# Kernel optimization log

Measured on AMD Instinct MI355X. Metric: run time of the kernel, lower is better.

Reference implementation:

```python
import jax, jax.numpy as jnp
import numpy as np

N, E, D, H, L, G = 50000, 800000, 128, 8, 3, 64
C = D // H  # per-head dim


def setup_inputs() -> dict:
    key = jax.random.key(0)
    ks = jax.random.split(key, 10)
    s = 1.0 / np.sqrt(D)  # glorot-ish scale
    return {
        "x": jax.random.normal(ks[0], (N, D), jnp.float32),
        "edge_index": jax.random.randint(ks[1], (2, E), 0, N, jnp.int32),
        "batch": jnp.sort(jax.random.randint(ks[2], (N,), 0, G, jnp.int32)),
        "Wq": jax.random.normal(ks[3], (L, D, D), jnp.float32) * s,
        "bq": jnp.zeros((L, D), jnp.float32),
        "Wk": jax.random.normal(ks[4], (L, D, D), jnp.float32) * s,
        "bk": jnp.zeros((L, D), jnp.float32),
        "Wv": jax.random.normal(ks[5], (L, D, D), jnp.float32) * s,
        "bv": jnp.zeros((L, D), jnp.float32),
        "Ws": jax.random.normal(ks[6], (L, D, D), jnp.float32) * s,
        "bs": jnp.zeros((L, D), jnp.float32),
        "w_gate": jax.random.normal(ks[7], (D, 1), jnp.float32) * s,
        "b_gate": jnp.zeros((1,), jnp.float32),
    }


def transformer_conv(x, src, dst, Wq, bq, Wk, bk, Wv, bv, Ws, bs):
    # PyG TransformerConv (concat=True, root_weight=True, no edge_attr, eval mode)
    n = x.shape[0]
    q = (x @ Wq + bq).reshape(n, H, C)
    k = (x @ Wk + bk).reshape(n, H, C)
    v = (x @ Wv + bv).reshape(n, H, C)
    # attention logits per edge: [E, H]
    alpha = jnp.einsum('ehc,ehc->eh', q[dst], k[src]) / np.sqrt(C).astype(np.float32)
    # segment softmax over incoming edges of each destination node
    amax = jax.ops.segment_max(alpha, dst, num_segments=n)          # [N, H]
    ea = jnp.exp(alpha - amax[dst])
    denom = jax.ops.segment_sum(ea, dst, num_segments=n)            # [N, H]
    attn = ea / (denom[dst] + 1e-16)                                # [E, H]
    msg = v[src] * attn[:, :, None]                                 # [E, H, C]
    out = jax.ops.segment_sum(msg, dst, num_segments=n).reshape(n, H * C)
    return out + x @ Ws + bs                                        # skip connection


def reference(x, edge_index, batch, Wq, bq, Wk, bk, Wv, bv, Ws, bs, w_gate, b_gate):
    src, dst = edge_index[0], edge_index[1]
    for l in range(L):
        x = transformer_conv(x, src, dst, Wq[l], bq[l], Wk[l], bk[l],
                             Wv[l], bv[l], Ws[l], bs[l])
    # ReadoutPhase: gated sum pool || max pool
    score = jax.nn.sigmoid(x @ w_gate + b_gate)                     # [N, 1]
    pool_sum = jax.ops.segment_sum(score * x, batch, num_segments=G)
    pool_max = jax.ops.segment_max(x, batch, num_segments=G)
    return jnp.concatenate([pool_sum, pool_max], axis=1)            # [G, 2D]
```

## Files before the change

### kernel.cpp

```cpp
#include <hip/hip_runtime.h>
#include <hip/hip_bf16.h>

#define NN 50000
#define EE 800000
#define GG 64
#define PCH 16
#define SCB ((NN + 255) / 256)

typedef __attribute__((ext_vector_type(8)))  short          s16x8;
typedef __attribute__((ext_vector_type(8)))  unsigned short u16x8;
typedef __attribute__((ext_vector_type(16))) float          f32x16;

union BFU { __hip_bfloat16 h; unsigned short u; };
__device__ __forceinline__ unsigned short f2bf(float f) {
    BFU b; b.h = __float2bfloat16(f); return b.u;
}
#define B2F_LO(u) __uint_as_float((u) << 16)
#define B2F_HI(u) __uint_as_float((u) & 0xffff0000u)
#define BF2F(us)  __uint_as_float(((unsigned)(us)) << 16)

__global__ __launch_bounds__(256) void hist_kernel(const int* __restrict__ dst,
                                                   int* __restrict__ counts) {
    int e = blockIdx.x * 256 + threadIdx.x;
    if (e < EE) atomicAdd(&counts[dst[e]], 1);
}

__global__ __launch_bounds__(256)
void block_scan(const int* __restrict__ counts, int* __restrict__ offsets,
                int* __restrict__ bsums) {
    __shared__ int sm[256];
    const int t = threadIdx.x;
    const int i = blockIdx.x * 256 + t;
    const int v = (i < NN) ? counts[i] : 0;
    sm[t] = v;
    __syncthreads();
    for (int off = 1; off < 256; off <<= 1) {
        int val = (t >= off) ? sm[t - off] : 0;
        __syncthreads();
        sm[t] += val;
        __syncthreads();
    }
    if (i < NN) offsets[i] = sm[t] - v;
    if (t == 255) bsums[blockIdx.x] = sm[255];
}

__global__ __launch_bounds__(256)
void scan_sums(int* __restrict__ bsums) {
    __shared__ int sm[256];
    const int t = threadIdx.x;
    const int v = (t < SCB) ? bsums[t] : 0;
    sm[t] = v;
    __syncthreads();
    for (int off = 1; off < 256; off <<= 1) {
        int val = (t >= off) ? sm[t - off] : 0;
        __syncthreads();
        sm[t] += val;
        __syncthreads();
    }
    if (t < SCB) bsums[t] = sm[t] - v;
}

__global__ __launch_bounds__(256)
void add_base(int* __restrict__ offsets, const int* __restrict__ bsums) {
    const int i = blockIdx.x * 256 + threadIdx.x;
    if (i < NN) offsets[i] += bsums[blockIdx.x];
    if (i == 0) offsets[NN] = EE;
}

__global__ __launch_bounds__(256) void scatter_kernel(const int* __restrict__ src,
                                                      const int* __restrict__ dst,
                                                      const int* __restrict__ offs,
                                                      int* __restrict__ cursor,
                                                      int* __restrict__ csrc) {
    int e = blockIdx.x * 256 + threadIdx.x;
    if (e < EE) {
        int dn = dst[e];
        int p = atomicAdd(&cursor[dn], 1);
        csrc[offs[dn] + p] = src[e];
    }
}

__global__ __launch_bounds__(256) void starts_kernel(const int* __restrict__ batch,
                                                     int* __restrict__ starts) {
    int i = blockIdx.x * 256 + threadIdx.x;
    if (i > NN) return;
    int b  = (i < NN) ? batch[i] : GG;
    int bp = (i == 0) ? -1 : batch[i - 1];
    for (int g = bp + 1; g <= b && g <= GG; ++g) starts[g] = i;
}

__global__ __launch_bounds__(256)
void deg_hist(const int* __restrict__ counts, int* __restrict__ dhist) {
    __shared__ int lh[256];
    const int t = threadIdx.x;
    lh[t] = 0;
    __syncthreads();
    const int i = blockIdx.x * 256 + t;
    if (i < NN) atomicAdd(&lh[min(counts[i], 255)], 1);
    __syncthreads();
    if (lh[t]) atomicAdd(&dhist[t], lh[t]);
}

__global__ __launch_bounds__(256)
void deg_scan(int* __restrict__ dhist) {
    __shared__ int sm[256];
    const int t = threadIdx.x;
    const int v = dhist[t];
    sm[t] = v;
    __syncthreads();
    for (int off = 1; off < 256; off <<= 1) {
        int val = (t >= off) ? sm[t - off] : 0;
        __syncthreads();
        sm[t] += val;
        __syncthreads();
    }
    dhist[t] = sm[t] - v;
}

__global__ __launch_bounds__(256)
void deg_scatter(const int* __restrict__ counts, const int* __restrict__ dbase,
                 int* __restrict__ dcur, int* __restrict__ perm) {
    __shared__ int lh[256];
    __shared__ int lb[256];
    const int t = threadIdx.x;
    lh[t] = 0;
    __syncthreads();
    const int i = blockIdx.x * 256 + t;
    int d = 0, r = 0;
    if (i < NN) {
        d = min(counts[i], 255);
        r = atomicAdd(&lh[d], 1);
    }
    __syncthreads();
    if (lh[t]) lb[t] = atomicAdd(&dcur[t], lh[t]);
    __syncthreads();
    if (i < NN) perm[dbase[d] + lb[d] + r] = i;
}

__global__ __launch_bounds__(256)
void prep_weights(const float* __restrict__ Wq, const float* __restrict__ Wk,
                  const float* __restrict__ Wv, const float* __restrict__ Ws,
                  unsigned short* __restrict__ wtbh, unsigned short* __restrict__ wtbl) {
    const int mat = blockIdx.x;
    const int l = mat >> 2, m = mat & 3;
    const float* W;
    switch (m) {
        case 0:  W = Wq; break;
        case 1:  W = Wk; break;
        case 2:  W = Wv; break;
        default: W = Ws; break;
    }
    W += (size_t)l * 16384;
    const int t = threadIdx.x;
    const int col = blockIdx.y * 16 + (t >> 4);
    const int kb  = (t & 15) * 8;
    u16x8 hi, lo;
    #pragma unroll
    for (int j = 0; j < 8; ++j) {
        float w = W[(kb + j) * 128 + col];
        unsigned short uh = f2bf(w);
        hi[j] = uh;
        lo[j] = f2bf(w - BF2F(uh));
    }
    const size_t o = (size_t)mat * 16384 + col * 128 + kb;
    *(u16x8*)(wtbh + o) = hi;
    *(u16x8*)(wtbl + o) = lo;
}

__global__ __launch_bounds__(256, 2)
void gemm_mfma(const float* __restrict__ xin,
               const unsigned short* __restrict__ wHg,
               const unsigned short* __restrict__ wLg,
               const float* __restrict__ bq, const float* __restrict__ bk,
               const float* __restrict__ bv, const float* __restrict__ bs,
               float* __restrict__ q, unsigned short* __restrict__ kvb,
               float* __restrict__ xs) {
    __shared__ unsigned short xl[16384];
    __shared__ unsigned short wsm[16384];
    const int t = threadIdx.x;
    const int n0 = blockIdx.x * 64;

    const float4* X4 = (const float4*)xin;
    for (int i = t; i < 1024; i += 256) {
        const int row = i >> 4, ch = i & 15;
        const int node = n0 + row;
        float4 fa = make_float4(0.f, 0.f, 0.f, 0.f);
        float4 fb = make_float4(0.f, 0.f, 0.f, 0.f);
        if (node < NN) { fa = X4[node * 32 + ch * 2]; fb = X4[node * 32 + ch * 2 + 1]; }
        const float fv[8] = {fa.x, fa.y, fa.z, fa.w, fb.x, fb.y, fb.z, fb.w};
        u16x8 hi, lo;
        #pragma unroll
        for (int j = 0; j < 8; ++j) {
            unsigned short uh = f2bf(fv[j]);
            hi[j] = uh;
            lo[j] = f2bf(fv[j] - BF2F(uh));
        }
        const int base = row * 128 + (ch ^ (row & 7)) * 8;
        *(u16x8*)&xl[base] = hi;
        *(u16x8*)&xl[8192 + base] = lo;
    }
    __syncthreads();

    const int lane = t & 63, wid = t >> 6;
    const int r = lane & 31, g = lane >> 5;
    const int nt = (wid & 1) * 32;
    const int cb = (wid >> 1) * 64;
    s16x8 ah[8], al[8];
    {
        const int row = nt + r;
        const int s = row & 7;
        const int rb = row * 128;
        #pragma unroll
        for (int kc = 0; kc < 8; ++kc) {
            const int idx = rb + (((kc << 1) | g) ^ s) * 8;
            ah[kc] = *(const s16x8*)&xl[idx];
            al[kc] = *(const s16x8*)&xl[8192 + idx];
        }
    }
    const int col0 = cb + r, col1 = cb + 32 + r;
    const int wb0 = col0 * 128, ws0 = col0 & 7;
    const int wb1 = col1 * 128, ws1 = col1 & 7;

    for (int m = 0; m < 4; ++m) {
        const bool split = (m == 0 || m == 3);
        f32x16 acc0, acc1;
        #pragma unroll
        for (int j = 0; j < 16; ++j) { acc0[j] = 0.f; acc1[j] = 0.f; }

        const int nparts = split ? 2 : 1;
        for (int part = 0; part < nparts; ++part) {
            __syncthreads();
            const u16x8* Wg = (const u16x8*)((part == 0 ? wHg : wLg) + m * 16384);
            for (int i = t; i < 2048; i += 256) {
                const int row = i >> 4, ch = i & 15;
                *(u16x8*)&wsm[row * 128 + (ch ^ (row & 7)) * 8] = Wg[i];
            }
            __syncthreads();
            #pragma unroll
            for (int kc = 0; kc < 8; ++kc) {
                const s16x8 b0 = *(const s16x8*)&wsm[wb0 + (((kc << 1) | g) ^ ws0) * 8];
                const s16x8 b1 = *(const s16x8*)&wsm[wb1 + (((kc << 1) | g) ^ ws1) * 8];
                acc0 = __builtin_amdgcn_mfma_f32_32x32x16_bf16(ah[kc], b0, acc0, 0, 0, 0);
                acc1 = __builtin_amdgcn_mfma_f32_32x32x16_bf16(ah[kc], b1, acc1, 0, 0, 0);
                if (split && part == 0) {
                    acc0 = __builtin_amdgcn_mfma_f32_32x32x16_bf16(al[kc], b0, acc0, 0, 0, 0);
                    acc1 = __builtin_amdgcn_mfma_f32_32x32x16_bf16(al[kc], b1, acc1, 0, 0, 0);
                }
            }
        }

        const float* bp;
        switch (m) {
            case 0:  bp = bq; break;
            case 1:  bp = bk; break;
            case 2:  bp = bv; break;
            default: bp = bs; break;
        }
        const float b0 = bp[col0], b1 = bp[col1];
        if (m == 0 || m == 3) {
            float* outp = (m == 0) ? q : xs;
            #pragma unroll
            for (int reg = 0; reg < 16; ++reg) {
                const int node = n0 + nt + (reg & 3) + 8 * (reg >> 2) + 4 * g;
                if (node < NN) {
                    outp[node * 128 + col0] = acc0[reg] + b0;
                    outp[node * 128 + col1] = acc1[reg] + b1;
                }
            }
        } else {
            const int koff = (m == 1) ? 0 : 16;
            const int o0 = (col0 >> 4) * 32 + koff + (col0 & 15);
            const int o1 = (col1 >> 4) * 32 + koff + (col1 & 15);
            #pragma unroll
            for (int reg = 0; reg < 16; ++reg) {
                const int node = n0 + nt + (reg & 3) + 8 * (reg >> 2) + 4 * g;
                if (node < NN) {
                    kvb[(size_t)node * 256 + o0] = f2bf(acc0[reg] + b0);
                    kvb[(size_t)node * 256 + o1] = f2bf(acc1[reg] + b1);
                }
            }
        }
    }
}

__global__ __launch_bounds__(256)
void attn_kernel(const float* __restrict__ q, const uint4* __restrict__ kv4,
                 float* __restrict__ xio,
                 const int* __restrict__ offs, const int* __restrict__ csrc,
                 const int* __restrict__ perm) {
    const int t = threadIdx.x;
    const int h = t & 7;
    const int quarter = (t >> 3) & 3;
    const int idx = blockIdx.x * 8 + (t >> 5);
    const int n = perm[idx];
    const float4* qp = (const float4*)(q + n * 128 + h * 16);
    const float4 q0 = qp[0], q1 = qp[1], q2 = qp[2], q3 = qp[3];
    float m = -__builtin_inff();
    float d = 0.f;
    float4 a0 = {}, a1 = {}, a2 = {}, a3 = {};
    const int e0 = offs[n], e1 = offs[n + 1];
    const int e = e0 + quarter;
    if (e < e1) {
        const uint4* kvp = kv4 + (size_t)csrc[e] * 32 + h * 4;
        uint4 ka = kvp[0], kb = kvp[1], va = kvp[2], vb = kvp[3];
        for (int en = e + 4;; en += 4) {
            uint4 nka, nkb, nva, nvb;
            const bool more = (en < e1);
            if (more) {
                const uint4* kvn = kv4 + (size_t)csrc[en] * 32 + h * 4;
                nka = kvn[0]; nkb = kvn[1]; nva = kvn[2]; nvb = kvn[3];
            }
            float dot =
                q0.x * B2F_LO(ka.x) + q0.y * B2F_HI(ka.x) + q0.z * B2F_LO(ka.y) + q0.w * B2F_HI(ka.y)
              + q1.x * B2F_LO(ka.z) + q1.y * B2F_HI(ka.z) + q1.z * B2F_LO(ka.w) + q1.w * B2F_HI(ka.w)
              + q2.x * B2F_LO(kb.x) + q2.y * B2F_HI(kb.x) + q2.z * B2F_LO(kb.y) + q2.w * B2F_HI(kb.y)
              + q3.x * B2F_LO(kb.z) + q3.y * B2F_HI(kb.z) + q3.z * B2F_LO(kb.w) + q3.w * B2F_HI(kb.w);
            const float alpha = dot * 0.25f;
            const float nm = fmaxf(m, alpha);
            const float scale = __expf(m - nm);
            const float p = __expf(alpha - nm);
            d = d * scale + p;
            a0.x = a0.x * scale + p * B2F_LO(va.x); a0.y = a0.y * scale + p * B2F_HI(va.x);
            a0.z = a0.z * scale + p * B2F_LO(va.y); a0.w = a0.w * scale + p * B2F_HI(va.y);
            a1.x = a1.x * scale + p * B2F_LO(va.z); a1.y = a1.y * scale + p * B2F_HI(va.z);
            a1.z = a1.z * scale + p * B2F_LO(va.w); a1.w = a1.w * scale + p * B2F_HI(va.w);
            a2.x = a2.x * scale + p * B2F_LO(vb.x); a2.y = a2.y * scale + p * B2F_HI(vb.x);
            a2.z = a2.z * scale + p * B2F_LO(vb.y); a2.w = a2.w * scale + p * B2F_HI(vb.y);
            a3.x = a3.x * scale + p * B2F_LO(vb.z); a3.y = a3.y * scale + p * B2F_HI(vb.z);
            a3.z = a3.z * scale + p * B2F_LO(vb.w); a3.w = a3.w * scale + p * B2F_HI(vb.w);
            m = nm;
            if (!more) break;
            ka = nka; kb = nkb; va = nva; vb = nvb;
        }
    }
    #pragma unroll
    for (int o = 8; o <= 16; o <<= 1) {
        const float mp = __shfl_xor(m, o);
        const float dp = __shfl_xor(d, o);
        const float mc = fmaxf(fmaxf(m, mp), -1e30f);
        const float s0 = __expf(m - mc);
        const float s1 = __expf(mp - mc);
        d = d * s0 + dp * s1;
        float pa;
        pa = __shfl_xor(a0.x, o); a0.x = a0.x * s0 + pa * s1;
        pa = __shfl_xor(a0.y, o); a0.y = a0.y * s0 + pa * s1;
        pa = __shfl_xor(a0.z, o); a0.z = a0.z * s0 + pa * s1;
        pa = __shfl_xor(a0.w, o); a0.w = a0.w * s0 + pa * s1;
        pa = __shfl_xor(a1.x, o); a1.x = a1.x * s0 + pa * s1;
        pa = __shfl_xor(a1.y, o); a1.y = a1.y * s0 + pa * s1;
        pa = __shfl_xor(a1.z, o); a1.z = a1.z * s0 + pa * s1;
        pa = __shfl_xor(a1.w, o); a1.w = a1.w * s0 + pa * s1;
        pa = __shfl_xor(a2.x, o); a2.x = a2.x * s0 + pa * s1;
        pa = __shfl_xor(a2.y, o); a2.y = a2.y * s0 + pa * s1;
        pa = __shfl_xor(a2.z, o); a2.z = a2.z * s0 + pa * s1;
        pa = __shfl_xor(a2.w, o); a2.w = a2.w * s0 + pa * s1;
        pa = __shfl_xor(a3.x, o); a3.x = a3.x * s0 + pa * s1;
        pa = __shfl_xor(a3.y, o); a3.y = a3.y * s0 + pa * s1;
        pa = __shfl_xor(a3.z, o); a3.z = a3.z * s0 + pa * s1;
        pa = __shfl_xor(a3.w, o); a3.w = a3.w * s0 + pa * s1;
        m = mc;
    }
    if (quarter == 0) {
        const float inv = 1.f / (d + 1e-16f);
        float4* op = (float4*)(xio + n * 128 + h * 16);
        float4 o0 = op[0], o1 = op[1], o2 = op[2], o3 = op[3];
        o0.x += a0.x * inv; o0.y += a0.y * inv; o0.z += a0.z * inv; o0.w += a0.w * inv;
        o1.x += a1.x * inv; o1.y += a1.y * inv; o1.z += a1.z * inv; o1.w += a1.w * inv;
        o2.x += a2.x * inv; o2.y += a2.y * inv; o2.z += a2.z * inv; o2.w += a2.w * inv;
        o3.x += a3.x * inv; o3.y += a3.y * inv; o3.z += a3.z * inv; o3.w += a3.w * inv;
        op[0] = o0; op[1] = o1; op[2] = o2; op[3] = o3;
    }
}

__global__ __launch_bounds__(128)
void pool_partial(const float* __restrict__ x, const float* __restrict__ wg,
                  const float* __restrict__ bg, const int* __restrict__ starts,
                  float* __restrict__ psum, float* __restrict__ pmax) {
    const int g  = blockIdx.x / PCH;
    const int ch = blockIdx.x % PCH;
    const int c  = threadIdx.x;
    const int s0 = starts[g], s1 = starts[g + 1];
    const int total = s1 - s0;
    const int len = (total + PCH - 1) / PCH;
    const int n0 = s0 + ch * len;
    const int n1 = min(n0 + len, s1);
    const float w = wg[c];
    const float b = bg[0];
    __shared__ float red[2];
    float sum = 0.f, mx = -__builtin_inff();
    for (int n = n0; n < n1; ++n) {
        const float xv = x[n * 128 + c];
        float p = xv * w;
        #pragma unroll
        for (int o = 32; o; o >>= 1) p += __shfl_xor(p, o);
        if ((c & 63) == 0) red[c >> 6] = p;
        __syncthreads();
        const float dot = red[0] + red[1];
        __syncthreads();
        const float score = 1.f / (1.f + __expf(-(dot + b)));
        sum += score * xv;
        mx = fmaxf(mx, xv);
    }
    psum[blockIdx.x * 128 + c] = sum;
    pmax[blockIdx.x * 128 + c] = mx;
}

__global__ __launch_bounds__(128)
void pool_final(const float* __restrict__ psum, const float* __restrict__ pmax,
                float* __restrict__ out) {
    const int g = blockIdx.x, c = threadIdx.x;
    float s = 0.f, m = -__builtin_inff();
    #pragma unroll
    for (int ch = 0; ch < PCH; ++ch) {
        s += psum[(g * PCH + ch) * 128 + c];
        m = fmaxf(m, pmax[(g * PCH + ch) * 128 + c]);
    }
    out[g * 256 + c] = s;
    out[g * 256 + 128 + c] = m;
}

extern "C" void kernel_launch(void* const* d_in, const int* in_sizes, int n_in,
                              void* d_out, int out_size, void* d_ws, size_t ws_size,
                              hipStream_t stream) {
    const float* x     = (const float*)d_in[0];
    const int*   ei    = (const int*)d_in[1];
    const int*   batch = (const int*)d_in[2];
    const float* Wq = (const float*)d_in[3];
    const float* bq = (const float*)d_in[4];
    const float* Wk = (const float*)d_in[5];
    const float* bk = (const float*)d_in[6];
    const float* Wv = (const float*)d_in[7];
    const float* bv = (const float*)d_in[8];
    const float* Ws = (const float*)d_in[9];
    const float* bs = (const float*)d_in[10];
    const float* wg = (const float*)d_in[11];
    const float* bg = (const float*)d_in[12];
    float* out = (float*)d_out;

    char* w = (char*)d_ws;
    float* qb            = (float*)w;          w += (size_t)NN * 128 * 4;
    unsigned short* kvb  = (unsigned short*)w; w += (size_t)NN * 256 * 2;
    float* bufA          = (float*)w;          w += (size_t)NN * 128 * 4;
    float* bufB          = (float*)w;          w += (size_t)NN * 128 * 4;
    float* psum          = (float*)w;          w += (size_t)GG * PCH * 128 * 4;
    float* pmax          = (float*)w;          w += (size_t)GG * PCH * 128 * 4;
    unsigned short* wtbh = (unsigned short*)w; w += (size_t)12 * 16384 * 2;
    unsigned short* wtbl = (unsigned short*)w; w += (size_t)12 * 16384 * 2;
    int* counts          = (int*)w;            w += (size_t)NN * 4;
    int* offsets         = (int*)w;            w += (size_t)(NN + 1) * 4;
    int* bsums           = (int*)w;            w += (size_t)256 * 4;
    int* dhist           = (int*)w;            w += (size_t)256 * 4;
    int* dcur            = (int*)w;            w += (size_t)256 * 4;
    int* perm            = (int*)w;            w += (size_t)NN * 4;
    int* csrc            = (int*)w;            w += (size_t)EE * 4;
    int* starts          = (int*)w;            w += (size_t)(GG + 1) * 4;

    const int* srcI = ei;
    const int* dstI = ei + EE;

    hipMemsetAsync(counts, 0, (size_t)NN * 4, stream);
    hipMemsetAsync(dhist, 0, 256 * 4, stream);
    hipMemsetAsync(dcur, 0, 256 * 4, stream);
    hist_kernel<<<(EE + 255) / 256, 256, 0, stream>>>(dstI, counts);
    block_scan<<<SCB, 256, 0, stream>>>(counts, offsets, bsums);
    scan_sums<<<1, 256, 0, stream>>>(bsums);
    add_base<<<SCB, 256, 0, stream>>>(offsets, bsums);
    deg_hist<<<SCB, 256, 0, stream>>>(counts, dhist);
    deg_scan<<<1, 256, 0, stream>>>(dhist);
    deg_scatter<<<SCB, 256, 0, stream>>>(counts, dhist, dcur, perm);
    hipMemsetAsync(counts, 0, (size_t)NN * 4, stream);
    scatter_kernel<<<(EE + 255) / 256, 256, 0, stream>>>(srcI, dstI, offsets, counts, csrc);
    starts_kernel<<<(NN + 256) / 256, 256, 0, stream>>>(batch, starts);
    prep_weights<<<dim3(12, 8), 256, 0, stream>>>(Wq, Wk, Wv, Ws, wtbh, wtbl);

    const float* xin = x;
    float* bufs[2] = {bufA, bufB};
    const int gemmBlocks = (NN + 63) / 64;
    const int attnBlocks = NN / 8;
    for (int l = 0; l < 3; ++l) {
        float* xs = bufs[l & 1];
        gemm_mfma<<<gemmBlocks, 256, 0, stream>>>(
            xin, wtbh + (size_t)l * 4 * 16384, wtbl + (size_t)l * 4 * 16384,
            bq + (size_t)l * 128, bk + (size_t)l * 128,
            bv + (size_t)l * 128, bs + (size_t)l * 128,
            qb, kvb, xs);
        attn_kernel<<<attnBlocks, 256, 0, stream>>>(qb, (const uint4*)kvb, xs, offsets, csrc, perm);
        xin = xs;
    }

    pool_partial<<<GG * PCH, 128, 0, stream>>>(xin, wg, bg, starts, psum, pmax);
    pool_final<<<GG, 128, 0, stream>>>(psum, pmax, out);
}
```

Baseline: 519.9 us.

## Load GEMM weight fragments directly from global memory, dropping LDS staging

```diff
diff --git a/kernel.cpp b/kernel.cpp
--- a/kernel.cpp
+++ b/kernel.cpp
@@ -140,7 +140,7 @@
 __global__ __launch_bounds__(256)
 void prep_weights(const float* __restrict__ Wq, const float* __restrict__ Wk,
                   const float* __restrict__ Wv, const float* __restrict__ Ws,
-                  unsigned short* __restrict__ wtbh, unsigned short* __restrict__ wtbl) {
+                  unsigned short* __restrict__ wfh, unsigned short* __restrict__ wfl) {
     const int mat = blockIdx.x;
     const int l = mat >> 2, m = mat & 3;
     const float* W;
@@ -153,21 +153,21 @@
     W += (size_t)l * 16384;
     const int t = threadIdx.x;
     const int col = blockIdx.y * 16 + (t >> 4);
-    const int kb  = (t & 15) * 8;
+    const int kk  = t & 15;
     u16x8 hi, lo;
     #pragma unroll
     for (int j = 0; j < 8; ++j) {
-        float w = W[(kb + j) * 128 + col];
+        float w = W[(kk * 8 + j) * 128 + col];
         unsigned short uh = f2bf(w);
         hi[j] = uh;
         lo[j] = f2bf(w - BF2F(uh));
     }
-    const size_t o = (size_t)mat * 16384 + col * 128 + kb;
-    *(u16x8*)(wtbh + o) = hi;
-    *(u16x8*)(wtbl + o) = lo;
-}
-
-__global__ __launch_bounds__(256, 2)
+    const size_t o = (size_t)mat * 16384 + ((size_t)kk * 128 + col) * 8;
+    *(u16x8*)(wfh + o) = hi;
+    *(u16x8*)(wfl + o) = lo;
+}
+
+__global__ __launch_bounds__(256)
 void gemm_mfma(const float* __restrict__ xin,
                const unsigned short* __restrict__ wHg,
                const unsigned short* __restrict__ wLg,
@@ -176,7 +176,6 @@
                float* __restrict__ q, unsigned short* __restrict__ kvb,
                float* __restrict__ xs) {
     __shared__ unsigned short xl[16384];
-    __shared__ unsigned short wsm[16384];
     const int t = threadIdx.x;
     const int n0 = blockIdx.x * 64;
 
@@ -218,34 +217,30 @@
         }
     }
     const int col0 = cb + r, col1 = cb + 32 + r;
-    const int wb0 = col0 * 128, ws0 = col0 & 7;
-    const int wb1 = col1 * 128, ws1 = col1 & 7;
-
+
+    #pragma unroll
     for (int m = 0; m < 4; ++m) {
         const bool split = (m == 0 || m == 3);
+        const unsigned short* WH = wHg + m * 16384;
+        const unsigned short* WL = wLg + m * 16384;
         f32x16 acc0, acc1;
         #pragma unroll
         for (int j = 0; j < 16; ++j) { acc0[j] = 0.f; acc1[j] = 0.f; }
 
-        const int nparts = split ? 2 : 1;
-        for (int part = 0; part < nparts; ++part) {
-            __syncthreads();
-            const u16x8* Wg = (const u16x8*)((part == 0 ? wHg : wLg) + m * 16384);
-            for (int i = t; i < 2048; i += 256) {
-                const int row = i >> 4, ch = i & 15;
-                *(u16x8*)&wsm[row * 128 + (ch ^ (row & 7)) * 8] = Wg[i];
-            }
-            __syncthreads();
-            #pragma unroll
-            for (int kc = 0; kc < 8; ++kc) {
-                const s16x8 b0 = *(const s16x8*)&wsm[wb0 + (((kc << 1) | g) ^ ws0) * 8];
-                const s16x8 b1 = *(const s16x8*)&wsm[wb1 + (((kc << 1) | g) ^ ws1) * 8];
-                acc0 = __builtin_amdgcn_mfma_f32_32x32x16_bf16(ah[kc], b0, acc0, 0, 0, 0);
-                acc1 = __builtin_amdgcn_mfma_f32_32x32x16_bf16(ah[kc], b1, acc1, 0, 0, 0);
-                if (split && part == 0) {
-                    acc0 = __builtin_amdgcn_mfma_f32_32x32x16_bf16(al[kc], b0, acc0, 0, 0, 0);
-                    acc1 = __builtin_amdgcn_mfma_f32_32x32x16_bf16(al[kc], b1, acc1, 0, 0, 0);
-                }
+        #pragma unroll
+        for (int kc = 0; kc < 8; ++kc) {
+            const int kk = (kc << 1) | g;
+            const s16x8 b0 = *(const s16x8*)&WH[(kk * 128 + col0) * 8];
+            const s16x8 b1 = *(const s16x8*)&WH[(kk * 128 + col1) * 8];
+            acc0 = __builtin_amdgcn_mfma_f32_32x32x16_bf16(ah[kc], b0, acc0, 0, 0, 0);
+            acc1 = __builtin_amdgcn_mfma_f32_32x32x16_bf16(ah[kc], b1, acc1, 0, 0, 0);
+            if (split) {
+                acc0 = __builtin_amdgcn_mfma_f32_32x32x16_bf16(al[kc], b0, acc0, 0, 0, 0);
+                acc1 = __builtin_amdgcn_mfma_f32_32x32x16_bf16(al[kc], b1, acc1, 0, 0, 0);
+                const s16x8 c0 = *(const s16x8*)&WL[(kk * 128 + col0) * 8];
+                const s16x8 c1 = *(const s16x8*)&WL[(kk * 128 + col1) * 8];
+                acc0 = __builtin_amdgcn_mfma_f32_32x32x16_bf16(ah[kc], c0, acc0, 0, 0, 0);
+                acc1 = __builtin_amdgcn_mfma_f32_32x32x16_bf16(ah[kc], c1, acc1, 0, 0, 0);
             }
         }
 
@@ -444,8 +439,8 @@
     float* bufB          = (float*)w;          w += (size_t)NN * 128 * 4;
     float* psum          = (float*)w;          w += (size_t)GG * PCH * 128 * 4;
     float* pmax          = (float*)w;          w += (size_t)GG * PCH * 128 * 4;
-    unsigned short* wtbh = (unsigned short*)w; w += (size_t)12 * 16384 * 2;
-    unsigned short* wtbl = (unsigned short*)w; w += (size_t)12 * 16384 * 2;
+    unsigned short* wfh  = (unsigned short*)w; w += (size_t)12 * 16384 * 2;
+    unsigned short* wfl  = (unsigned short*)w; w += (size_t)12 * 16384 * 2;
     int* counts          = (int*)w;            w += (size_t)NN * 4;
     int* offsets         = (int*)w;            w += (size_t)(NN + 1) * 4;
     int* bsums           = (int*)w;            w += (size_t)256 * 4;
@@ -471,7 +466,7 @@
     hipMemsetAsync(counts, 0, (size_t)NN * 4, stream);
     scatter_kernel<<<(EE + 255) / 256, 256, 0, stream>>>(srcI, dstI, offsets, counts, csrc);
     starts_kernel<<<(NN + 256) / 256, 256, 0, stream>>>(batch, starts);
-    prep_weights<<<dim3(12, 8), 256, 0, stream>>>(Wq, Wk, Wv, Ws, wtbh, wtbl);
+    prep_weights<<<dim3(12, 8), 256, 0, stream>>>(Wq, Wk, Wv, Ws, wfh, wfl);
 
     const float* xin = x;
     float* bufs[2] = {bufA, bufB};
@@ -480,7 +475,7 @@
     for (int l = 0; l < 3; ++l) {
         float* xs = bufs[l & 1];
         gemm_mfma<<<gemmBlocks, 256, 0, stream>>>(
-            xin, wtbh + (size_t)l * 4 * 16384, wtbl + (size_t)l * 4 * 16384,
+            xin, wfh + (size_t)l * 4 * 16384, wfl + (size_t)l * 4 * 16384,
             bq + (size_t)l * 128, bk + (size_t)l * 128,
             bv + (size_t)l * 128, bs + (size_t)l * 128,
             qb, kvb, xs);
```

New measurement: 479.2 us. 1.08x faster.
